# Kernel tuning notes

Measured on AMD Instinct MI355X. Metric: run time of the kernel, lower is better.

## Reference

```python
import jax, jax.numpy as jnp
import numpy as np

N, E, F_IN, H, HEADS, L = 50000, 800000, 64, 64, 4, 5
NEG_SLOPE = 0.2  # PyG GATv2 default negative_slope


def _gatv2(h, src, dst, Wl, bl, Wr, br, att, bias, n):
    # PyG GATv2Conv, concat=False: x_l = lin_l(x), x_r = lin_r(x)
    xl = (h @ Wl + bl).reshape(n, HEADS, H)
    xr = (h @ Wr + br).reshape(n, HEADS, H)
    # per-edge score: a^T LeakyReLU(x_l[src] + x_r[dst])  -> [E', heads]
    z = jax.nn.leaky_relu(xl[src] + xr[dst], NEG_SLOPE)
    e = jnp.einsum('ehc,hc->eh', z, att)
    # segment softmax over incoming edges of each dst node
    m = jax.lax.stop_gradient(jax.ops.segment_max(e, dst, num_segments=n))
    ex = jnp.exp(e - m[dst])
    s = jax.ops.segment_sum(ex, dst, num_segments=n)
    alpha = ex / s[dst]
    out = jax.ops.segment_sum(xl[src] * alpha[:, :, None], dst, num_segments=n)
    return out.mean(axis=1) + bias  # concat=False -> mean over heads, + bias


def _forward(node_features, Wl, bl, Wr, br, att, gat_bias,
             Wm1, bm1, Wm2, bm2, Wp, bp, Wv1, bv1, Wv2, bv2,
             src, dst, current_pos, valid_neighbors, owned_nodes):
    n = node_features.shape[0]
    h = node_features
    for i in range(L):  # depth = 5 since N > 15
        h_new = jax.nn.elu(_gatv2(h, src, dst, Wl[i], bl[i], Wr[i], br[i], att[i], gat_bias[i], n))
        h = h_new if i == 0 else h + h_new  # residual after first layer
    cand = jnp.concatenate([jnp.asarray([current_pos], dtype=valid_neighbors.dtype), valid_neighbors])
    curr = h[current_pos]
    pairs = jnp.concatenate([jnp.broadcast_to(curr, (cand.shape[0], curr.shape[0])), h[cand]], axis=1)
    move_logits = (jax.nn.relu(pairs @ Wm1 + bm1) @ Wm2 + bm2)[:, 0]
    price_logits = h[owned_nodes] @ Wp + bp
    g = jnp.concatenate([h.mean(axis=0), curr])
    value = (jax.nn.relu(g @ Wv1 + bv1) @ Wv2 + bv2)[0]
    return move_logits, price_logits, value


def setup_inputs() -> dict:
    key = jax.random.key(0)
    ks = jax.random.split(key, 24)
    s = 0.05
    return {
        'node_features': jax.random.normal(ks[0], (N, F_IN), jnp.float32),
        'edge_index': jax.random.randint(ks[1], (2, E), 0, N),
        'current_pos': 7,
        'valid_neighbors': jax.random.randint(ks[2], (8,), 0, N),
        'owned_nodes': jax.random.randint(ks[3], (10,), 0, N),
        'Wl': jax.random.normal(ks[4], (L, F_IN, HEADS * H), jnp.float32) * s,
        'bl': jnp.zeros((L, HEADS * H), jnp.float32),
        'Wr': jax.random.normal(ks[5], (L, F_IN, HEADS * H), jnp.float32) * s,
        'br': jnp.zeros((L, HEADS * H), jnp.float32),
        'att': jax.random.normal(ks[6], (L, HEADS, H), jnp.float32) * s,
        'gat_bias': jnp.zeros((L, H), jnp.float32),
        'Wm1': jax.random.normal(ks[7], (2 * H, 128), jnp.float32) * s,
        'bm1': jnp.zeros((128,), jnp.float32),
        'Wm2': jax.random.normal(ks[8], (128, 1), jnp.float32) * s,
        'bm2': jnp.zeros((1,), jnp.float32),
        'Wp': jax.random.normal(ks[9], (H, 3), jnp.float32) * s,
        'bp': jnp.zeros((3,), jnp.float32),
        'Wv1': jax.random.normal(ks[10], (2 * H, 64), jnp.float32) * s,
        'bv1': jnp.zeros((64,), jnp.float32),
        'Wv2': jax.random.normal(ks[11], (64, 1), jnp.float32) * s,
        'bv2': jnp.zeros((1,), jnp.float32),
    }


def reference(node_features, edge_index, current_pos, valid_neighbors, owned_nodes,
              Wl, bl, Wr, br, att, gat_bias, Wm1, bm1, Wm2, bm2, Wp, bp, Wv1, bv1, Wv2, bv2):
    n = node_features.shape[0]
    loops = jnp.arange(n, dtype=edge_index.dtype)  # add_self_loops=True
    src = jnp.concatenate([edge_index[0], loops])
    dst = jnp.concatenate([edge_index[1], loops])
    return _forward(node_features, Wl, bl, Wr, br, att, gat_bias,
                    Wm1, bm1, Wm2, bm2, Wp, bp, Wv1, bv1, Wv2, bv2,
                    src, dst, current_pos, valid_neighbors, owned_nodes)
```

## Files before the change

### kernel.cpp

```cpp
#include <hip/hip_runtime.h>
#include <hip/hip_bf16.h>
#include <hip/hip_fp16.h>

#define NHID 256
#define HDIM 64
#define HEADS 4
#define LAYERS 5
#define LOG2E 1.4426950408889634f

using half8 = __attribute__((ext_vector_type(8))) _Float16;
using f32x4 = __attribute__((ext_vector_type(4))) float;

__global__ void count_deg(const int* __restrict__ dst, int* __restrict__ counts, int E, int n) {
    int i = blockIdx.x * blockDim.x + threadIdx.x;
    if (i < E) atomicAdd(&counts[dst[i]], 1);
    else if (i < E + n) atomicAdd(&counts[i - E], 1);
}

__global__ __launch_bounds__(256) void scan_partial(const int* __restrict__ counts,
                                                    int* __restrict__ out,
                                                    int* __restrict__ partials, int n) {
    __shared__ int buf[256];
    int tid = threadIdx.x;
    int i = blockIdx.x * 256 + tid;
    int v = (i < n) ? counts[i] : 0;
    buf[tid] = v;
    __syncthreads();
    for (int o = 1; o < 256; o <<= 1) {
        int t = (tid >= o) ? buf[tid - o] : 0;
        __syncthreads();
        buf[tid] += t;
        __syncthreads();
    }
    if (i < n) out[i] = buf[tid] - v;
    if (tid == 255) partials[blockIdx.x] = buf[255];
}

__global__ __launch_bounds__(256) void scan_partials_scan(int* __restrict__ partials,
                                                          int* __restrict__ out,
                                                          int nblk, int n) {
    __shared__ int buf[256];
    int tid = threadIdx.x;
    int v = (tid < nblk) ? partials[tid] : 0;
    buf[tid] = v;
    __syncthreads();
    for (int o = 1; o < 256; o <<= 1) {
        int t = (tid >= o) ? buf[tid - o] : 0;
        __syncthreads();
        buf[tid] += t;
        __syncthreads();
    }
    if (tid < nblk) partials[tid] = buf[tid] - v;
    if (tid == 255) out[n] = buf[255];
}

__global__ __launch_bounds__(256) void scan_add_offsets(int* __restrict__ out,
                                                        const int* __restrict__ partials, int n) {
    int i = blockIdx.x * 256 + threadIdx.x;
    if (i < n) out[i] += partials[blockIdx.x];
}

__global__ void copy_i32(const int* __restrict__ a, int* __restrict__ b, int n) {
    int i = blockIdx.x * blockDim.x + threadIdx.x;
    if (i < n) b[i] = a[i];
}

__global__ void scatter_edges(const int* __restrict__ src, const int* __restrict__ dst,
                              int* __restrict__ row_fill, int* __restrict__ col_src, int E, int n) {
    int i = blockIdx.x * blockDim.x + threadIdx.x;
    if (i < E) {
        int p = atomicAdd(&row_fill[dst[i]], 1);
        col_src[p] = src[i];
    } else if (i < E + n) {
        int node = i - E;
        int p = atomicAdd(&row_fill[node], 1);
        col_src[p] = node;
    }
}

__global__ __launch_bounds__(256) void wprep(const float* __restrict__ Wl,
                                             const float* __restrict__ Wr,
                                             __half* __restrict__ Wfrag) {
    int layer = blockIdx.x >> 4;
    int idx = (blockIdx.x & 15) * 256 + threadIdx.x;
    int t = idx >> 7, kh = (idx >> 6) & 1, lane = idx & 63;
    const float* WlL = Wl + (size_t)layer * 64 * 256;
    const float* WrL = Wr + (size_t)layer * 64 * 256;
    int col = t * 16 + (lane & 15);
    __half* outp = Wfrag + (size_t)layer * 32768 + ((size_t)(t * 2 + kh) * 64 + lane) * 8;
#pragma unroll
    for (int j = 0; j < 8; ++j) {
        int k = kh * 32 + (lane >> 4) * 8 + j;
        float v = (col < 256) ? WlL[k * 256 + col] : WrL[k * 256 + (col - 256)];
        outp[j] = __float2half(v);
    }
}

__global__ void conv_h16(const float* __restrict__ h, __half* __restrict__ h16, int total) {
    int i = blockIdx.x * blockDim.x + threadIdx.x;
    if (i < total) h16[i] = __float2half(h[i]);
}

__global__ __launch_bounds__(256) void gemm_mfma(const __half* __restrict__ h16,
                                                 const __half* __restrict__ Wfrag,
                                                 const float* __restrict__ bl,
                                                 const float* __restrict__ br,
                                                 __half* __restrict__ xlh,
                                                 float* __restrict__ xr, int n) {
    int w = threadIdx.x >> 6, l = threadIdx.x & 63;
    int row0 = blockIdx.x * 64 + w * 16;
    if (row0 >= n) return;
    int arow = row0 + (l & 15);
    half8 A0 = *(const half8*)(h16 + (size_t)arow * 64 + (l >> 4) * 8);
    half8 A1 = *(const half8*)(h16 + (size_t)arow * 64 + 32 + (l >> 4) * 8);
    int orow = row0 + (l >> 4) * 4;
#pragma unroll
    for (int t = 0; t < 32; ++t) {
        half8 B0 = *(const half8*)(Wfrag + ((size_t)(t * 2 + 0) * 64 + l) * 8);
        half8 B1 = *(const half8*)(Wfrag + ((size_t)(t * 2 + 1) * 64 + l) * 8);
        f32x4 acc = {0.f, 0.f, 0.f, 0.f};
        acc = __builtin_amdgcn_mfma_f32_16x16x32_f16(A0, B0, acc, 0, 0, 0);
        acc = __builtin_amdgcn_mfma_f32_16x16x32_f16(A1, B1, acc, 0, 0, 0);
        int col = t * 16 + (l & 15);
        if (col < 256) {
            float b = bl[col];
#pragma unroll
            for (int j = 0; j < 4; ++j)
                xlh[(size_t)(orow + j) * 256 + col] = __float2half(acc[j] + b);
        } else {
            float b = br[col - 256];
#pragma unroll
            for (int j = 0; j < 4; ++j)
                xr[(size_t)(orow + j) * 256 + (col - 256)] = acc[j] + b;
        }
    }
}

template <int CTRL>
__device__ __forceinline__ float dpp_mov_f32(float x) {
    return __int_as_float(__builtin_amdgcn_update_dpp(0, __float_as_int(x), CTRL, 0xf, 0xf, false));
}
__device__ __forceinline__ float group16_reduce_add(float x) {
    x += dpp_mov_f32<0xB1>(x);
    x += dpp_mov_f32<0x4E>(x);
    x += dpp_mov_f32<0x124>(x);
    x += dpp_mov_f32<0x128>(x);
    return x;
}

__global__ __launch_bounds__(256) void gat_node(const __half* __restrict__ xlh,
                                                const float* __restrict__ xr,
                                                const int* __restrict__ row_ptr,
                                                const int* __restrict__ col_src,
                                                const float* __restrict__ att,
                                                const float* __restrict__ gbias,
                                                const float* __restrict__ h_res,
                                                float* __restrict__ h_out,
                                                __half* __restrict__ h16_out, int n) {
    int wid  = threadIdx.x >> 6;
    int lane = threadIdx.x & 63;
    int node = blockIdx.x * 4 + wid;
    if (node >= n) return;

    const uint2* xl2 = (const uint2*)xlh;
    float4 xrv = ((const float4*)(xr + (size_t)node * NHID))[lane];
    float4 av  = ((const float4*)att)[lane];
    float4 av06 = make_float4(av.x * (0.6f * LOG2E), av.y * (0.6f * LOG2E),
                              av.z * (0.6f * LOG2E), av.w * (0.6f * LOG2E));
    float4 av04 = make_float4(av.x * (0.4f * LOG2E), av.y * (0.4f * LOG2E),
                              av.z * (0.4f * LOG2E), av.w * (0.4f * LOG2E));

    float  m = -INFINITY, s = 0.f;
    float4 acc = make_float4(0.f, 0.f, 0.f, 0.f);

    int e0 = row_ptr[node], e1 = row_ptr[node + 1];
    uint2 xa = xl2[(size_t)(unsigned)col_src[e0] * 64 + lane];
    uint2 xb = xl2[(size_t)(unsigned)col_src[e0 + 1] * 64 + lane];

    for (int idx = e0; idx < e1; ++idx) {
        uint2 raw = xa;
        xa = xb;
        xb = xl2[(size_t)(unsigned)col_src[idx + 2] * 64 + lane];

        float2 f0 = __half22float2(*(const __half2*)&raw.x);
        float2 f1 = __half22float2(*(const __half2*)&raw.y);
        float4 cur = make_float4(f0.x, f0.y, f1.x, f1.y);

        float z0 = cur.x + xrv.x;
        float z1 = cur.y + xrv.y;
        float z2 = cur.z + xrv.z;
        float z3 = cur.w + xrv.w;
        float pp;
        pp = fmaf(av06.x, z0, av04.x * fabsf(z0));
        pp = fmaf(av06.y, z1, fmaf(av04.y, fabsf(z1), pp));
        pp = fmaf(av06.z, z2, fmaf(av04.z, fabsf(z2), pp));
        pp = fmaf(av06.w, z3, fmaf(av04.w, fabsf(z3), pp));
        pp = group16_reduce_add(pp);

        if (__any(pp > m + 11.541560f)) {
            float mn = fmaxf(m, pp);
            float f  = exp2f(m - mn);
            float w  = exp2f(pp - mn);
            acc.x = acc.x * f + w * cur.x;
            acc.y = acc.y * f + w * cur.y;
            acc.z = acc.z * f + w * cur.z;
            acc.w = acc.w * f + w * cur.w;
            s = s * f + w;
            m = mn;
        } else {
            float w = exp2f(pp - m);
            acc.x += w * cur.x;
            acc.y += w * cur.y;
            acc.z += w * cur.z;
            acc.w += w * cur.w;
            s += w;
        }
    }

    float inv = 1.0f / s;
    float4 v = make_float4(acc.x * inv, acc.y * inv, acc.z * inv, acc.w * inv);
    v.x += __shfl_xor(v.x, 16, 64); v.y += __shfl_xor(v.y, 16, 64);
    v.z += __shfl_xor(v.z, 16, 64); v.w += __shfl_xor(v.w, 16, 64);
    v.x += __shfl_xor(v.x, 32, 64); v.y += __shfl_xor(v.y, 32, 64);
    v.z += __shfl_xor(v.z, 32, 64); v.w += __shfl_xor(v.w, 32, 64);

    if (lane < 16) {
        float4 g = ((const float4*)gbias)[lane];
        float4 o;
        o.x = v.x * 0.25f + g.x;
        o.y = v.y * 0.25f + g.y;
        o.z = v.z * 0.25f + g.z;
        o.w = v.w * 0.25f + g.w;
        o.x = (o.x > 0.f) ? o.x : expm1f(o.x);
        o.y = (o.y > 0.f) ? o.y : expm1f(o.y);
        o.z = (o.z > 0.f) ? o.z : expm1f(o.z);
        o.w = (o.w > 0.f) ? o.w : expm1f(o.w);
        if (h_res) {
            float4 r = ((const float4*)(h_res + (size_t)node * 64))[lane];
            o.x += r.x; o.y += r.y; o.z += r.z; o.w += r.w;
        }
        ((float4*)(h_out + (size_t)node * 64))[lane] = o;
        __half2 p0 = __float22half2_rn(make_float2(o.x, o.y));
        __half2 p1 = __float22half2_rn(make_float2(o.z, o.w));
        uint2 pk;
        pk.x = *(unsigned*)&p0;
        pk.y = *(unsigned*)&p1;
        ((uint2*)(h16_out + (size_t)node * 64))[lane] = pk;
    }
}

__global__ __launch_bounds__(256) void col_sum(const float* __restrict__ h,
                                               float* __restrict__ gsum, int n) {
    int col = threadIdx.x & 63;
    int sub = threadIdx.x >> 6;
    float s = 0.f;
    for (int r = blockIdx.x * 4 + sub; r < n; r += gridDim.x * 4)
        s += h[(size_t)r * 64 + col];
    __shared__ float tmp[4][64];
    tmp[sub][col] = s;
    __syncthreads();
    if (threadIdx.x < 64) {
        int t = threadIdx.x;
        atomicAdd(&gsum[t], tmp[0][t] + tmp[1][t] + tmp[2][t] + tmp[3][t]);
    }
}

__global__ __launch_bounds__(128) void heads_kernel(const float* __restrict__ h,
                                                    const float* __restrict__ gsum,
                                                    const int* __restrict__ cur_pos,
                                                    const int* __restrict__ valid,
                                                    const int* __restrict__ owned,
                                                    const float* __restrict__ Wm1, const float* __restrict__ bm1,
                                                    const float* __restrict__ Wm2, const float* __restrict__ bm2,
                                                    const float* __restrict__ Wp,  const float* __restrict__ bp,
                                                    const float* __restrict__ Wv1, const float* __restrict__ bv1,
                                                    const float* __restrict__ Wv2, const float* __restrict__ bv2,
                                                    float* __restrict__ out, int n) {
    int blk = blockIdx.x;
    int tid = threadIdx.x;
    int pos = cur_pos[0];

    if (blk < 9) {
        int cand = (blk == 0) ? pos : valid[blk - 1];
        const float* hcur  = h + (size_t)pos  * 64;
        const float* hcand = h + (size_t)cand * 64;
        float a = bm1[tid];
#pragma unroll
        for (int k = 0; k < 64; ++k) a += hcur[k]  * Wm1[k * 128 + tid];
#pragma unroll
        for (int k = 0; k < 64; ++k) a += hcand[k] * Wm1[(64 + k) * 128 + tid];
        a = fmaxf(a, 0.f) * Wm2[tid];
#pragma unroll
        for (int o = 1; o < 64; o <<= 1) a += __shfl_xor(a, o, 64);
        __shared__ float red[2];
        if ((tid & 63) == 0) red[tid >> 6] = a;
        __syncthreads();
        if (tid == 0) out[blk] = red[0] + red[1] + bm2[0];
    } else if (blk == 9) {
        if (tid < 30) {
            int i = tid / 3, cc = tid % 3;
            int node = owned[i];
            const float* hn = h + (size_t)node * 64;
            float a = bp[cc];
#pragma unroll
            for (int k = 0; k < 64; ++k) a += hn[k] * Wp[k * 3 + cc];
            out[9 + tid] = a;
        }
    } else {
        float invn = 1.0f / (float)n;
        const float* hcur = h + (size_t)pos * 64;
        float a = 0.f;
        if (tid < 64) {
            a = bv1[tid];
#pragma unroll
            for (int k = 0; k < 64; ++k) a += (gsum[k] * invn) * Wv1[k * 64 + tid];
#pragma unroll
            for (int k = 0; k < 64; ++k) a += hcur[k] * Wv1[(64 + k) * 64 + tid];
            a = fmaxf(a, 0.f) * Wv2[tid];
#pragma unroll
            for (int o = 1; o < 64; o <<= 1) a += __shfl_xor(a, o, 64);
            if (tid == 0) out[39] = a + bv2[0];
        }
    }
}

extern "C" void kernel_launch(void* const* d_in, const int* in_sizes, int n_in,
                              void* d_out, int out_size, void* d_ws, size_t ws_size,
                              hipStream_t stream) {
    const float* nf    = (const float*)d_in[0];
    const int*   ei    = (const int*)d_in[1];
    const int*   cpos  = (const int*)d_in[2];
    const int*   valid = (const int*)d_in[3];
    const int*   owned = (const int*)d_in[4];
    const float* Wl    = (const float*)d_in[5];
    const float* bl    = (const float*)d_in[6];
    const float* Wr    = (const float*)d_in[7];
    const float* br    = (const float*)d_in[8];
    const float* att   = (const float*)d_in[9];
    const float* gbias = (const float*)d_in[10];
    const float* Wm1 = (const float*)d_in[11];
    const float* bm1 = (const float*)d_in[12];
    const float* Wm2 = (const float*)d_in[13];
    const float* bm2 = (const float*)d_in[14];
    const float* Wp  = (const float*)d_in[15];
    const float* bp  = (const float*)d_in[16];
    const float* Wv1 = (const float*)d_in[17];
    const float* bv1 = (const float*)d_in[18];
    const float* Wv2 = (const float*)d_in[19];
    const float* bv2 = (const float*)d_in[20];
    float* out = (float*)d_out;

    int n = in_sizes[0] / 64;
    int E = in_sizes[1] / 2;
    const int* srcp = ei;
    const int* dstp = ei + E;

    char* w = (char*)d_ws;
    auto alloc = [&](size_t bytes) -> char* {
        char* p = w;
        w += (bytes + 255) & ~(size_t)255;
        return p;
    };
    __half* xlh     = (__half*)alloc((size_t)n * NHID * 2);
    float* xr       = (float*)alloc((size_t)n * NHID * 4);
    float* hA       = (float*)alloc((size_t)n * 64 * 4);
    float* hB       = (float*)alloc((size_t)n * 64 * 4);
    __half* h16     = (__half*)alloc((size_t)n * 64 * 2);
    __half* Wfrag   = (__half*)alloc((size_t)LAYERS * 32768 * 2);
    float* gsum     = (float*)alloc(64 * 4);
    int*   row_ptr  = (int*)alloc((size_t)(n + 1) * 4);
    int*   row_fill = (int*)alloc((size_t)n * 4);
    int*   col_src  = (int*)alloc((size_t)(E + n + 8) * 4);
    int*   partials = (int*)alloc(256 * 4);

    int nblk = (n + 255) / 256;
    int nthr = E + n;

    hipMemsetAsync(row_fill, 0, (size_t)n * 4, stream);
    count_deg<<<(nthr + 255) / 256, 256, 0, stream>>>(dstp, row_fill, E, n);
    scan_partial<<<nblk, 256, 0, stream>>>(row_fill, row_ptr, partials, n);
    scan_partials_scan<<<1, 256, 0, stream>>>(partials, row_ptr, nblk, n);
    scan_add_offsets<<<nblk, 256, 0, stream>>>(row_ptr, partials, n);
    copy_i32<<<(n + 255) / 256, 256, 0, stream>>>(row_ptr, row_fill, n);
    scatter_edges<<<(nthr + 255) / 256, 256, 0, stream>>>(srcp, dstp, row_fill, col_src, E, n);
    hipMemsetAsync(col_src + E + n, 0, 8 * 4, stream);

    wprep<<<LAYERS * 16, 256, 0, stream>>>(Wl, Wr, Wfrag);
    conv_h16<<<(n * 64 + 255) / 256, 256, 0, stream>>>(nf, h16, n * 64);

    const float* hin = nf;
    float* hnext = hB;
    for (int i = 0; i < LAYERS; ++i) {
        gemm_mfma<<<(n + 63) / 64, 256, 0, stream>>>(h16, Wfrag + (size_t)i * 32768,
                                                     bl + i * 256, br + i * 256,
                                                     xlh, xr, n);
        const float* res = (i == 0) ? nullptr : hin;
        float* outp = (i == 0) ? hA : hnext;
        gat_node<<<(n + 3) / 4, 256, 0, stream>>>(xlh, xr, row_ptr, col_src,
                                                  att + i * HEADS * 64, gbias + i * 64,
                                                  res, outp, h16, n);
        if (i == 0) {
            hin = hA; hnext = hB;
        } else {
            const float* t = hin;
            hin = outp;
            hnext = (float*)t;
        }
    }

    hipMemsetAsync(gsum, 0, 64 * 4, stream);
    col_sum<<<256, 256, 0, stream>>>(hin, gsum, n);
    heads_kernel<<<11, 128, 0, stream>>>(hin, gsum, cpos, valid, owned,
                                         Wm1, bm1, Wm2, bm2, Wp, bp,
                                         Wv1, bv1, Wv2, bv2, out, n);
}
```

Before: 754.3 us.

## Store x_r in fp16, compute GATv2 scores with packed half math, pre-shift indices

The right projection x_r is now written by the GEMM as fp16 instead of fp32, which halves its write and read traffic. The edge-score loop adds and applies LeakyReLU with packed fp16 vector ops (max(z, 0.2z)) rather than converting to float and using the abs-based formula. Source indices in the CSR are stored pre-multiplied by the row byte stride (<<9), so the gather address costs less arithmetic, and the scan-offset and copy kernels are merged into one launch. Computing the scores in fp16 lowers precision, and the shifted indices limit node ids to about 4M.

```diff
diff --git a/kernel.cpp b/kernel.cpp
--- a/kernel.cpp
+++ b/kernel.cpp
@@ -9,6 +9,7 @@
 #define LOG2E 1.4426950408889634f
 
 using half8 = __attribute__((ext_vector_type(8))) _Float16;
+using h2    = __attribute__((ext_vector_type(2))) _Float16;
 using f32x4 = __attribute__((ext_vector_type(4))) float;
 
 __global__ void count_deg(const int* __restrict__ dst, int* __restrict__ counts, int E, int n) {
@@ -54,15 +55,15 @@
     if (tid == 255) out[n] = buf[255];
 }
 
-__global__ __launch_bounds__(256) void scan_add_offsets(int* __restrict__ out,
-                                                        const int* __restrict__ partials, int n) {
+__global__ __launch_bounds__(256) void scan_add_offsets2(int* __restrict__ out,
+                                                         int* __restrict__ out2,
+                                                         const int* __restrict__ partials, int n) {
     int i = blockIdx.x * 256 + threadIdx.x;
-    if (i < n) out[i] += partials[blockIdx.x];
-}
-
-__global__ void copy_i32(const int* __restrict__ a, int* __restrict__ b, int n) {
-    int i = blockIdx.x * blockDim.x + threadIdx.x;
-    if (i < n) b[i] = a[i];
+    if (i < n) {
+        int v = out[i] + partials[blockIdx.x];
+        out[i] = v;
+        out2[i] = v;
+    }
 }
 
 __global__ void scatter_edges(const int* __restrict__ src, const int* __restrict__ dst,
@@ -70,11 +71,11 @@
     int i = blockIdx.x * blockDim.x + threadIdx.x;
     if (i < E) {
         int p = atomicAdd(&row_fill[dst[i]], 1);
-        col_src[p] = src[i];
+        col_src[p] = src[i] << 9;
     } else if (i < E + n) {
         int node = i - E;
         int p = atomicAdd(&row_fill[node], 1);
-        col_src[p] = node;
+        col_src[p] = node << 9;
     }
 }
 
@@ -106,7 +107,7 @@
                                                  const float* __restrict__ bl,
                                                  const float* __restrict__ br,
                                                  __half* __restrict__ xlh,
-                                                 float* __restrict__ xr, int n) {
+                                                 __half* __restrict__ xrh, int n) {
     int w = threadIdx.x >> 6, l = threadIdx.x & 63;
     int row0 = blockIdx.x * 64 + w * 16;
     if (row0 >= n) return;
@@ -131,7 +132,7 @@
             float b = br[col - 256];
 #pragma unroll
             for (int j = 0; j < 4; ++j)
-                xr[(size_t)(orow + j) * 256 + (col - 256)] = acc[j] + b;
+                xrh[(size_t)(orow + j) * 256 + (col - 256)] = __float2half(acc[j] + b);
         }
     }
 }
@@ -149,7 +150,7 @@
 }
 
 __global__ __launch_bounds__(256) void gat_node(const __half* __restrict__ xlh,
-                                                const float* __restrict__ xr,
+                                                const __half* __restrict__ xrh,
                                                 const int* __restrict__ row_ptr,
                                                 const int* __restrict__ col_src,
                                                 const float* __restrict__ att,
@@ -162,57 +163,59 @@
     int node = blockIdx.x * 4 + wid;
     if (node >= n) return;
 
-    const uint2* xl2 = (const uint2*)xlh;
-    float4 xrv = ((const float4*)(xr + (size_t)node * NHID))[lane];
-    float4 av  = ((const float4*)att)[lane];
-    float4 av06 = make_float4(av.x * (0.6f * LOG2E), av.y * (0.6f * LOG2E),
-                              av.z * (0.6f * LOG2E), av.w * (0.6f * LOG2E));
-    float4 av04 = make_float4(av.x * (0.4f * LOG2E), av.y * (0.4f * LOG2E),
-                              av.z * (0.4f * LOG2E), av.w * (0.4f * LOG2E));
-
-    float  m = -INFINITY, s = 0.f;
+    const char* xlb = (const char*)xlh;
+    int laneoff = lane << 3;
+
+    uint2 xrp = ((const uint2*)(xrh + (size_t)node * NHID))[lane];
+    h2 xr01 = __builtin_bit_cast(h2, xrp.x);
+    h2 xr23 = __builtin_bit_cast(h2, xrp.y);
+
+    float4 av = ((const float4*)att)[lane];
+    av.x *= LOG2E; av.y *= LOG2E; av.z *= LOG2E; av.w *= LOG2E;
+    h2 c02 = {(_Float16)0.2f, (_Float16)0.2f};
+
+    float m = -INFINITY, s = 0.f;
     float4 acc = make_float4(0.f, 0.f, 0.f, 0.f);
 
     int e0 = row_ptr[node], e1 = row_ptr[node + 1];
-    uint2 xa = xl2[(size_t)(unsigned)col_src[e0] * 64 + lane];
-    uint2 xb = xl2[(size_t)(unsigned)col_src[e0 + 1] * 64 + lane];
+    uint2 xa = *(const uint2*)(xlb + (size_t)(unsigned)col_src[e0] + laneoff);
+    uint2 xb = *(const uint2*)(xlb + (size_t)(unsigned)col_src[e0 + 1] + laneoff);
 
     for (int idx = e0; idx < e1; ++idx) {
         uint2 raw = xa;
         xa = xb;
-        xb = xl2[(size_t)(unsigned)col_src[idx + 2] * 64 + lane];
-
-        float2 f0 = __half22float2(*(const __half2*)&raw.x);
-        float2 f1 = __half22float2(*(const __half2*)&raw.y);
-        float4 cur = make_float4(f0.x, f0.y, f1.x, f1.y);
-
-        float z0 = cur.x + xrv.x;
-        float z1 = cur.y + xrv.y;
-        float z2 = cur.z + xrv.z;
-        float z3 = cur.w + xrv.w;
+        xb = *(const uint2*)(xlb + (size_t)(unsigned)col_src[idx + 2] + laneoff);
+
+        h2 cur01 = __builtin_bit_cast(h2, raw.x);
+        h2 cur23 = __builtin_bit_cast(h2, raw.y);
+        h2 z01 = cur01 + xr01;
+        h2 z23 = cur23 + xr23;
+        z01 = __builtin_elementwise_max(z01, z01 * c02);
+        z23 = __builtin_elementwise_max(z23, z23 * c02);
+
         float pp;
-        pp = fmaf(av06.x, z0, av04.x * fabsf(z0));
-        pp = fmaf(av06.y, z1, fmaf(av04.y, fabsf(z1), pp));
-        pp = fmaf(av06.z, z2, fmaf(av04.z, fabsf(z2), pp));
-        pp = fmaf(av06.w, z3, fmaf(av04.w, fabsf(z3), pp));
+        pp = (float)z01.x * av.x;
+        pp = fmaf((float)z01.y, av.y, pp);
+        pp = fmaf((float)z23.x, av.z, pp);
+        pp = fmaf((float)z23.y, av.w, pp);
         pp = group16_reduce_add(pp);
 
         if (__any(pp > m + 11.541560f)) {
             float mn = fmaxf(m, pp);
             float f  = exp2f(m - mn);
             float w  = exp2f(pp - mn);
-            acc.x = acc.x * f + w * cur.x;
-            acc.y = acc.y * f + w * cur.y;
-            acc.z = acc.z * f + w * cur.z;
-            acc.w = acc.w * f + w * cur.w;
+            acc.x = fmaf((float)cur01.x, w, acc.x * f);
+            acc.y = fmaf((float)cur01.y, w, acc.y * f);
+            acc.z = fmaf((float)cur23.x, w, acc.z * f);
+            acc.w = fmaf((float)cur23.y, w, acc.w * f);
             s = s * f + w;
             m = mn;
         } else {
             float w = exp2f(pp - m);
-            acc.x += w * cur.x;
-            acc.y += w * cur.y;
-            acc.z += w * cur.z;
-            acc.w += w * cur.w;
+            acc.x = fmaf((float)cur01.x, w, acc.x);
+            acc.y = fmaf((float)cur01.y, w, acc.y);
+            acc.z = fmaf((float)cur23.x, w, acc.z);
+            acc.w = fmaf((float)cur23.y, w, acc.w);
             s += w;
         }
     }
@@ -362,7 +365,7 @@
         return p;
     };
     __half* xlh     = (__half*)alloc((size_t)n * NHID * 2);
-    float* xr       = (float*)alloc((size_t)n * NHID * 4);
+    __half* xrh     = (__half*)alloc((size_t)n * NHID * 2);
     float* hA       = (float*)alloc((size_t)n * 64 * 4);
     float* hB       = (float*)alloc((size_t)n * 64 * 4);
     __half* h16     = (__half*)alloc((size_t)n * 64 * 2);
@@ -380,8 +383,7 @@
     count_deg<<<(nthr + 255) / 256, 256, 0, stream>>>(dstp, row_fill, E, n);
     scan_partial<<<nblk, 256, 0, stream>>>(row_fill, row_ptr, partials, n);
     scan_partials_scan<<<1, 256, 0, stream>>>(partials, row_ptr, nblk, n);
-    scan_add_offsets<<<nblk, 256, 0, stream>>>(row_ptr, partials, n);
-    copy_i32<<<(n + 255) / 256, 256, 0, stream>>>(row_ptr, row_fill, n);
+    scan_add_offsets2<<<nblk, 256, 0, stream>>>(row_ptr, row_fill, partials, n);
     scatter_edges<<<(nthr + 255) / 256, 256, 0, stream>>>(srcp, dstp, row_fill, col_src, E, n);
     hipMemsetAsync(col_src + E + n, 0, 8 * 4, stream);
 
@@ -393,10 +395,10 @@
     for (int i = 0; i < LAYERS; ++i) {
         gemm_mfma<<<(n + 63) / 64, 256, 0, stream>>>(h16, Wfrag + (size_t)i * 32768,
                                                      bl + i * 256, br + i * 256,
-                                                     xlh, xr, n);
+                                                     xlh, xrh, n);
         const float* res = (i == 0) ? nullptr : hin;
         float* outp = (i == 0) ? hA : hnext;
-        gat_node<<<(n + 3) / 4, 256, 0, stream>>>(xlh, xr, row_ptr, col_src,
+        gat_node<<<(n + 3) / 4, 256, 0, stream>>>(xlh, xrh, row_ptr, col_src,
                                                   att + i * HEADS * 64, gbias + i * 64,
                                                   res, outp, h16, n);
         if (i == 0) {
```

New measurement: 746.9 us. About the same (-1.0%).
